# Kernel optimization log

Hardware: AMD Instinct MI355X
Metric: run time of the kernel (lower is better)

## Reference

```python
import jax, jax.numpy as jnp
import numpy as np

ALPHA1 = 0.5
ALPHA2 = 0.5
EXP_WEIGHTED = False
N = 16384


def setup_inputs() -> dict:
    key = jax.random.key(0)
    k1, k2 = jax.random.split(key)
    inp = jax.random.normal(k1, (N,), dtype=jnp.float32)
    tgt = jax.random.uniform(k2, (N,), dtype=jnp.float32)
    return {"input": inp, "target": tgt}


def reference(input, target):
    n = input.shape[0]
    # mask[i, j] = target[j] > target[i]  (pairs where j is ranked above i)
    mask = target[None, :] > target[:, None]  # [N, N] bool
    # BPR term: log(1 + exp(-(input[j] - input[i]))) == softplus(input[i] - input[j])
    bpr = jax.nn.softplus(input[:, None] - input[None, :])  # [N, N]
    # MSE term depends only on row i, broadcast over j
    mse = (input - target) ** 2  # [N]
    x = ALPHA1 * bpr + ALPHA2 * mse[:, None]  # [N, N]
    if EXP_WEIGHTED:
        w = jnp.expm1(target)  # exp(target) - 1
        x = w[:, None] * w[None, :] * x
    # x[x < 0] = 0, and only masked pairs contribute
    x = jnp.where(mask, jnp.maximum(x, 0.0), 0.0)
    total = jnp.sum(x)
    if EXP_WEIGHTED:
        scale = 2.0 / (n * (jnp.e - 1.0)) ** 2
    else:
        scale = 2.0 / n ** 2
    return scale * total
```

## Files before the change

kernel.cpp:

```cpp
#include <hip/hip_runtime.h>


#define N_ELEM 16384
#define NBUCK  4096
#define CHUNK  256
#define NPAIR  208
#define TPB    10
#define NBLK   209
#define PF     0xAAAAAAAAu

__device__ __forceinline__ float fexp2(float x){ return __builtin_amdgcn_exp2f(x); }
__device__ __forceinline__ float flog2(float x){ return __builtin_amdgcn_logf(x); }

__global__ __launch_bounds__(1024) void fused_kernel(
    const float* __restrict__ input, const float* __restrict__ target,
    float* __restrict__ wsA, int* __restrict__ cntA, int* __restrict__ gdone,
    float* __restrict__ out)
{
    const float L2E   = 1.4426950408889634f;
    const float INVN2 = 1.0f / (16384.0f * 16384.0f);
    const int b = blockIdx.x, tid = threadIdx.x, lane = tid & 63;
    const int wu = __builtin_amdgcn_readfirstlane((int)(threadIdx.x >> 6));

    __shared__ int histLds[NBUCK];
    __shared__ __align__(16) float cLds[CHUNK];
    __shared__ float wsLds[16];
    __shared__ int   wtot[16];

    float vsum = 0.0f;

    if (b == NPAIR) {
        for (int q = tid; q < NBUCK; q += 1024) histLds[q] = 0;
        __syncthreads();
        int packed[16];
        #pragma unroll
        for (int q = 0; q < 16; ++q) {
            const int idx = (q << 10) + tid;
            const float t = target[idx];
            int bk = (int)(t * 4096.0f);
            bk = bk < 0 ? 0 : (bk > 4095 ? 4095 : bk);
            const int ticket = atomicAdd(&histLds[bk], 1);
            packed[q] = (bk << 15) | ticket;
        }
        __syncthreads();
        int v[4], le[4]; int s = 0;
        #pragma unroll
        for (int q = 0; q < 4; ++q) v[q] = histLds[4 * tid + q];
        #pragma unroll
        for (int q = 0; q < 4; ++q) { le[q] = s; s += v[q]; }
        int inc = s;
        #pragma unroll
        for (int d = 1; d < 64; d <<= 1) {
            int n = __shfl_up(inc, d, 64); if (lane >= d) inc += n;
        }
        if (lane == 63) wtot[wu] = inc;
        __syncthreads();
        int woff = 0;
        #pragma unroll
        for (int w = 0; w < 16; ++w) woff += (w < wu) ? wtot[w] : 0;
        const int texcl = woff + (inc - s);
        #pragma unroll
        for (int q = 0; q < 4; ++q) histLds[4 * tid + q] = texcl + le[q];
        __syncthreads();
        #pragma unroll
        for (int q = 0; q < 16; ++q) {
            const int idx = (q << 10) + tid;
            const int pos = histLds[packed[q] >> 15] + (packed[q] & 0x7FFF);
            const float x = input[idx], t = target[idx];
            const float d = x - t;
            vsum += (-x * (float)pos + d * d * (float)(16383 - pos)) * INVN2;
        }
    } else {
        const int u0 = b * TPB;
        int cj = (int)((sqrtf(8.0f * (float)u0 + 1.0f) - 1.0f) * 0.5f);
        while ((cj + 1) * (cj + 2) / 2 <= u0) ++cj;
        while (cj * (cj + 1) / 2 > u0) --cj;
        int ci = u0 - cj * (cj + 1) / 2;

        float la0 = 0.0f, la1 = 0.0f;
        int cjCur = -1;
        for (int m = 0; m < TPB; ++m) {
            if (cj != cjCur) {
                __syncthreads();
                if (tid < CHUNK) cLds[tid] = fexp2(input[cj * CHUNK + tid] * L2E);
                cjCur = cj;
                __syncthreads();
            }
            float Xr[4];
            #pragma unroll
            for (int k = 0; k < 4; ++k)
                Xr[k] = fexp2(input[ci * CHUNK + 64 * k + lane] * L2E);
            const float4* __restrict__ cp4 = (const float4*)(cLds + wu * 16);

            if (ci != cj) {
                #pragma unroll
                for (int jj = 0; jj < 2; ++jj) {
                    const float4 A = cp4[2*jj+0], B = cp4[2*jj+1];
                    #pragma unroll
                    for (int k = 0; k < 4; ++k) {
                        const float X = Xr[k];
                        float p = (X + A.x) * (X + A.y);
                        p *= (X + A.z) * (X + A.w);
                        p *= (X + B.x) * (X + B.y);
                        p *= (X + B.z) * (X + B.w);
                        if (k & 1) la1 += flog2(p); else la0 += flog2(p);
                    }
                }
            } else {
                #pragma unroll
                for (int jj = 0; jj < 2; ++jj) {
                    const float4 A = cp4[2*jj+0], B = cp4[2*jj+1];
                    const int jb = wu * 16 + jj * 8;
                    #pragma unroll
                    for (int k = 0; k < 4; ++k) {
                        const float X = Xr[k];
                        const int rr = 64 * k + lane;
                        float p = 1.0f;
                        p *= (jb + 0 > rr) ? (X + A.x) : 1.0f;
                        p *= (jb + 1 > rr) ? (X + A.y) : 1.0f;
                        p *= (jb + 2 > rr) ? (X + A.z) : 1.0f;
                        p *= (jb + 3 > rr) ? (X + A.w) : 1.0f;
                        p *= (jb + 4 > rr) ? (X + B.x) : 1.0f;
                        p *= (jb + 5 > rr) ? (X + B.y) : 1.0f;
                        p *= (jb + 6 > rr) ? (X + B.z) : 1.0f;
                        p *= (jb + 7 > rr) ? (X + B.w) : 1.0f;
                        if (k & 1) la1 += flog2(p); else la0 += flog2(p);
                    }
                }
            }
            if (ci == cj) { ++cj; ci = 0; } else { ++ci; }
        }
        vsum = (la0 + la1) * (0.6931471805599453f * INVN2);
    }

    #pragma unroll
    for (int off = 32; off; off >>= 1) vsum += __shfl_down(vsum, off, 64);
    if (lane == 0) wsLds[wu] = vsum;
    __syncthreads();

    if (wu == 0) {
        float s = (lane < 16) ? wsLds[lane] : 0.0f;
        #pragma unroll
        for (int off = 8; off; off >>= 1) s += __shfl_down(s, off, 64);
        int isFinal = 0;
        if (lane == 0) {
            const int g = b & 63;
            float* slot  = wsA  + 32 * g;
            int*   cslot = cntA + 32 * g;
            const float old = __hip_atomic_fetch_add(slot, s,
                __ATOMIC_RELAXED, __HIP_MEMORY_SCOPE_AGENT);
            asm volatile("s_waitcnt vmcnt(0)" :: "v"(old) : "memory");
            const unsigned tkt = (unsigned)__hip_atomic_fetch_add(cslot, 1,
                __ATOMIC_RELAXED, __HIP_MEMORY_SCOPE_AGENT) - PF;
            const unsigned gsz = (g < 17) ? 4u : 3u;
            if (tkt == gsz - 1u) {
                asm volatile("s_waitcnt vmcnt(0)" ::: "memory");
                const unsigned gd = (unsigned)__hip_atomic_fetch_add(gdone, 1,
                    __ATOMIC_RELAXED, __HIP_MEMORY_SCOPE_AGENT) - PF;
                isFinal = (gd == 63u);
            }
        }
        isFinal = __shfl(isFinal, 0, 64);
        if (isFinal) {
            float v = __hip_atomic_fetch_add(wsA + 32 * lane, 0.0f,
                __ATOMIC_RELAXED, __HIP_MEMORY_SCOPE_AGENT);
            #pragma unroll
            for (int off = 32; off; off >>= 1) v += __shfl_down(v, off, 64);
            if (lane == 0)
                out[0] = v - 64.0f * __uint_as_float(PF);
        }
    }
}

extern "C" void kernel_launch(void* const* d_in, const int* in_sizes, int n_in,
                              void* d_out, int out_size, void* d_ws, size_t ws_size,
                              hipStream_t stream) {
    const float* input  = (const float*)d_in[0];
    const float* target = (const float*)d_in[1];
    float* out   = (float*)d_out;
    int*   wsi   = (int*)d_ws;
    int*   gdone = wsi + 8;
    float* wsA   = (float*)d_ws + 32768;
    int*   cntA  = wsi + 65536;

    fused_kernel<<<NBLK, 1024, 0, stream>>>(input, target, wsA, cntA, gdone, out);
}
```

Before: 70.42 us.

## Spread tile work over more blocks and halve log count via 16-term products

The grid grows from 209 to 512 blocks, with each block taking 4 or 5 triangle tiles instead of 10, so the pairwise work is spread across more compute units. Each block now holds 16 columns per wave in registers and multiplies 16 (X+C) factors before each log2, halving the number of transcendental calls. To keep these longer products from overflowing, both exponentials are pre-scaled by 0.5 and the missing ln2 per factor is added back through a per-thread pair count. The per-group ticket threshold becomes 8, to match the new block count. The launch-bounds occupancy hint and larger products may raise register pressure, and extreme inputs could lose precision or overflow.

```diff
diff --git a/kernel.cpp b/kernel.cpp
--- a/kernel.cpp
+++ b/kernel.cpp
@@ -4,15 +4,14 @@
 #define N_ELEM 16384
 #define NBUCK  4096
 #define CHUNK  256
-#define NPAIR  208
-#define TPB    10
-#define NBLK   209
+#define NPAIR  511
+#define NBLK   512
 #define PF     0xAAAAAAAAu
 
 __device__ __forceinline__ float fexp2(float x){ return __builtin_amdgcn_exp2f(x); }
 __device__ __forceinline__ float flog2(float x){ return __builtin_amdgcn_logf(x); }
 
-__global__ __launch_bounds__(1024) void fused_kernel(
+__global__ __launch_bounds__(1024, 8) void fused_kernel(
     const float* __restrict__ input, const float* __restrict__ target,
     float* __restrict__ wsA, int* __restrict__ cntA, int* __restrict__ gdone,
     float* __restrict__ out)
@@ -71,66 +70,67 @@
             vsum += (-x * (float)pos + d * d * (float)(16383 - pos)) * INVN2;
         }
     } else {
-        const int u0 = b * TPB;
+        const int ntb = (b < 475) ? 4 : 5;
+        const int u0  = (b < 475) ? (b << 2) : (1900 + 5 * (b - 475));
         int cj = (int)((sqrtf(8.0f * (float)u0 + 1.0f) - 1.0f) * 0.5f);
         while ((cj + 1) * (cj + 2) / 2 <= u0) ++cj;
         while (cj * (cj + 1) / 2 > u0) --cj;
         int ci = u0 - cj * (cj + 1) / 2;
 
         float la0 = 0.0f, la1 = 0.0f;
-        int cjCur = -1;
-        for (int m = 0; m < TPB; ++m) {
+        int   cnt = 0;
+        int   cjCur = -1;
+        for (int m = 0; m < ntb; ++m) {
             if (cj != cjCur) {
                 __syncthreads();
-                if (tid < CHUNK) cLds[tid] = fexp2(input[cj * CHUNK + tid] * L2E);
+                if (tid < CHUNK)
+                    cLds[tid] = 0.5f * fexp2(input[cj * CHUNK + tid] * L2E);
                 cjCur = cj;
                 __syncthreads();
             }
-            float Xr[4];
+            float Xh[4];
             #pragma unroll
             for (int k = 0; k < 4; ++k)
-                Xr[k] = fexp2(input[ci * CHUNK + 64 * k + lane] * L2E);
+                Xh[k] = 0.5f * fexp2(input[ci * CHUNK + 64 * k + lane] * L2E);
             const float4* __restrict__ cp4 = (const float4*)(cLds + wu * 16);
+            const float4 A = cp4[0], B = cp4[1], C = cp4[2], D = cp4[3];
 
             if (ci != cj) {
                 #pragma unroll
-                for (int jj = 0; jj < 2; ++jj) {
-                    const float4 A = cp4[2*jj+0], B = cp4[2*jj+1];
-                    #pragma unroll
-                    for (int k = 0; k < 4; ++k) {
-                        const float X = Xr[k];
-                        float p = (X + A.x) * (X + A.y);
-                        p *= (X + A.z) * (X + A.w);
-                        p *= (X + B.x) * (X + B.y);
-                        p *= (X + B.z) * (X + B.w);
-                        if (k & 1) la1 += flog2(p); else la0 += flog2(p);
-                    }
+                for (int k = 0; k < 4; ++k) {
+                    const float X = Xh[k];
+                    float p = (X + A.x) * (X + A.y);
+                    p *= (X + A.z) * (X + A.w);
+                    p *= (X + B.x) * (X + B.y);
+                    p *= (X + B.z) * (X + B.w);
+                    p *= (X + C.x) * (X + C.y);
+                    p *= (X + C.z) * (X + C.w);
+                    p *= (X + D.x) * (X + D.y);
+                    p *= (X + D.z) * (X + D.w);
+                    if (k & 1) la1 += flog2(p); else la0 += flog2(p);
                 }
+                cnt += 64;
             } else {
+                const int jb = wu * 16;
                 #pragma unroll
-                for (int jj = 0; jj < 2; ++jj) {
-                    const float4 A = cp4[2*jj+0], B = cp4[2*jj+1];
-                    const int jb = wu * 16 + jj * 8;
-                    #pragma unroll
-                    for (int k = 0; k < 4; ++k) {
-                        const float X = Xr[k];
-                        const int rr = 64 * k + lane;
-                        float p = 1.0f;
-                        p *= (jb + 0 > rr) ? (X + A.x) : 1.0f;
-                        p *= (jb + 1 > rr) ? (X + A.y) : 1.0f;
-                        p *= (jb + 2 > rr) ? (X + A.z) : 1.0f;
-                        p *= (jb + 3 > rr) ? (X + A.w) : 1.0f;
-                        p *= (jb + 4 > rr) ? (X + B.x) : 1.0f;
-                        p *= (jb + 5 > rr) ? (X + B.y) : 1.0f;
-                        p *= (jb + 6 > rr) ? (X + B.z) : 1.0f;
-                        p *= (jb + 7 > rr) ? (X + B.w) : 1.0f;
-                        if (k & 1) la1 += flog2(p); else la0 += flog2(p);
-                    }
+                for (int k = 0; k < 4; ++k) {
+                    const float X = Xh[k];
+                    const int rr = 64 * k + lane;
+                    float p = 1.0f; int c = 0;
+                    #define PRD(col, q) do { const bool ok = (jb + (q)) > rr;   \
+                        p *= ok ? (X + (col)) : 1.0f; c += ok ? 1 : 0; } while (0)
+                    PRD(A.x,0);  PRD(A.y,1);  PRD(A.z,2);  PRD(A.w,3);
+                    PRD(B.x,4);  PRD(B.y,5);  PRD(B.z,6);  PRD(B.w,7);
+                    PRD(C.x,8);  PRD(C.y,9);  PRD(C.z,10); PRD(C.w,11);
+                    PRD(D.x,12); PRD(D.y,13); PRD(D.z,14); PRD(D.w,15);
+                    #undef PRD
+                    if (k & 1) la1 += flog2(p); else la0 += flog2(p);
+                    cnt += c;
                 }
             }
             if (ci == cj) { ++cj; ci = 0; } else { ++ci; }
         }
-        vsum = (la0 + la1) * (0.6931471805599453f * INVN2);
+        vsum = (la0 + la1 + (float)cnt) * (0.6931471805599453f * INVN2);
     }
 
     #pragma unroll
@@ -152,8 +152,7 @@
             asm volatile("s_waitcnt vmcnt(0)" :: "v"(old) : "memory");
             const unsigned tkt = (unsigned)__hip_atomic_fetch_add(cslot, 1,
                 __ATOMIC_RELAXED, __HIP_MEMORY_SCOPE_AGENT) - PF;
-            const unsigned gsz = (g < 17) ? 4u : 3u;
-            if (tkt == gsz - 1u) {
+            if (tkt == 7u) {
                 asm volatile("s_waitcnt vmcnt(0)" ::: "memory");
                 const unsigned gd = (unsigned)__hip_atomic_fetch_add(gdone, 1,
                     __ATOMIC_RELAXED, __HIP_MEMORY_SCOPE_AGENT) - PF;
```

After: 73.04 us. +3.7%, slower.
